# Kernel optimization log

Measured on AMD Instinct MI355X. Metric: run time of the kernel, lower is better.

The kernel has to match this reference:

```python
import jax, jax.numpy as jnp
import numpy as np

# DAttentionBaseline config (matches init_kwargs)
NH, HC, G = 8, 32, 4          # n_heads, n_head_channels, n_groups
ORF = 2.0                      # offset_range_factor
KK = 5                         # offset conv kernel (stage_idx=2)


def _conv1x1(x, w, b=None):
    # x: (B,C,H,W), w: (O,C)
    y = jnp.einsum('bchw,oc->bohw', x, w)
    return y if b is None else y + b[None, :, None, None]


def _ref_points(Hk, Wk, dtype):
    # replicates torch.meshgrid(..., indexing='xy') as in the source
    ly = jnp.linspace(0.5, Hk - 0.5, Hk, dtype=dtype)
    lx = jnp.linspace(0.5, Wk - 0.5, Wk, dtype=dtype)
    ry, rx = jnp.meshgrid(ly, lx, indexing='xy')  # shapes (Wk, Hk); Hk==Wk here
    return jnp.stack([ry / Hk * 2 - 1, rx / Wk * 2 - 1], axis=-1)  # (Hk,Wk,2)


def _grid_sample(img, grid):
    # bilinear, align_corners=True, zero padding. img:(N,C,Hi,Wi), grid:(N,Hg,Wg,2) in [-1,1] (x,y)
    N, C, Hi, Wi = img.shape
    gx = (grid[..., 0] + 1.0) * 0.5 * (Wi - 1)
    gy = (grid[..., 1] + 1.0) * 0.5 * (Hi - 1)
    x0 = jnp.floor(gx); y0 = jnp.floor(gy)
    x1 = x0 + 1.0;      y1 = y0 + 1.0
    wx1 = gx - x0; wx0 = 1.0 - wx1
    wy1 = gy - y0; wy0 = 1.0 - wy1
    nidx = jnp.arange(N)[:, None, None]

    def gather(yf, xf):
        valid = (xf >= 0) & (xf <= Wi - 1) & (yf >= 0) & (yf <= Hi - 1)
        xi = jnp.clip(xf, 0, Wi - 1).astype(jnp.int32)
        yi = jnp.clip(yf, 0, Hi - 1).astype(jnp.int32)
        vals = img[nidx, :, yi, xi]  # (N,Hg,Wg,C)
        return vals * valid[..., None].astype(img.dtype)

    out = (gather(y0, x0) * (wy0 * wx0)[..., None]
           + gather(y0, x1) * (wy0 * wx1)[..., None]
           + gather(y1, x0) * (wy1 * wx0)[..., None]
           + gather(y1, x1) * (wy1 * wx1)[..., None])
    return out.transpose(0, 3, 1, 2)  # (N,C,Hg,Wg)


def _forward(x, wq, bq, w_off_dw, b_off_dw, ln_g, ln_b, w_off_pj, wk, bk, wv, bv, wo, bo, rpe_table):
    B, C, H, W = x.shape
    GC = C // G            # group channels
    GH = NH // G           # group heads
    scale = HC ** -0.5

    q = _conv1x1(x, wq, bq)                                   # (B,C,H,W)
    q_off = q.reshape(B * G, GC, H, W)

    # conv_offset: depthwise conv -> LayerNorm over channels -> GELU -> 1x1 conv to 2
    off = jax.lax.conv_general_dilated(
        q_off, w_off_dw, (1, 1), [(KK // 2, KK // 2), (KK // 2, KK // 2)],
        feature_group_count=GC, dimension_numbers=('NCHW', 'OIHW', 'NCHW'))
    off = off + b_off_dw[None, :, None, None]
    mu = off.mean(axis=1, keepdims=True)
    var = off.var(axis=1, keepdims=True)
    off = (off - mu) * jax.lax.rsqrt(var + 1e-5)
    off = off * ln_g[None, :, None, None] + ln_b[None, :, None, None]
    off = jax.nn.gelu(off, approximate=False)
    offset = jnp.einsum('bchw,oc->bohw', off, w_off_pj)       # (B*G,2,Hk,Wk)

    Hk, Wk = offset.shape[2], offset.shape[3]
    ns = Hk * Wk
    rng = jnp.array([1.0 / Hk, 1.0 / Wk], dtype=x.dtype).reshape(1, 2, 1, 1)
    offset = jnp.tanh(offset) * rng * ORF                     # offset_range_factor > 0
    offset = offset.transpose(0, 2, 3, 1)                     # (B*G,Hk,Wk,2)

    ref = _ref_points(Hk, Wk, x.dtype)                        # (Hk,Wk,2)
    pos = offset + ref[None]                                  # (B*G,Hk,Wk,2), (y,x) order

    xs = _grid_sample(x.reshape(B * G, GC, H, W), pos[..., ::-1])  # (B*G,GC,Hk,Wk)
    xs = xs.reshape(B, C, 1, ns)

    k = _conv1x1(xs, wk, bk).reshape(B * NH, HC, ns)
    v = _conv1x1(xs, wv, bv).reshape(B * NH, HC, ns)
    qf = q.reshape(B * NH, HC, H * W)
    attn = jnp.einsum('bcm,bcn->bmn', qf, k) * scale          # (B*NH, HW, ns)

    # RPE via grid_sample on the (2H-1, 2W-1) bias table
    rpe = jnp.broadcast_to(rpe_table[None], (B,) + rpe_table.shape)
    rpe = rpe.reshape(B * G, GH, 2 * H - 1, 2 * W - 1)
    qg = _ref_points(H, W, x.dtype).reshape(H * W, 2)
    disp = (qg[None, :, None, :] - pos.reshape(B * G, ns, 2)[:, None, :, :]) * 0.5  # (B*G,HW,ns,2)
    bias = _grid_sample(rpe, disp[..., ::-1]).reshape(B * NH, H * W, ns)
    attn = attn + bias

    attn = jax.nn.softmax(attn, axis=2)
    out = jnp.einsum('bmn,bcn->bcm', attn, v).reshape(B, C, H, W)
    y = _conv1x1(out, wo, bo)
    return (y,
            pos.reshape(B, G, Hk, Wk, 2),
            jnp.broadcast_to(ref[None, None], (B, G, Hk, Wk, 2)))


def setup_inputs() -> dict:
    key = jax.random.key(0)
    ks = jax.random.split(key, 8)
    B, C, H, W = 4, 256, 32, 32
    GC = C // G
    s = 0.02

    def n(k, shape, sc=s):
        return jax.random.normal(k, shape, jnp.float32) * sc

    return {
        'x': jax.random.normal(ks[0], (B, C, H, W), jnp.float32),
        'wq': n(ks[1], (C, C)), 'bq': jnp.zeros((C,), jnp.float32),
        'w_off_dw': n(ks[2], (GC, 1, KK, KK)), 'b_off_dw': jnp.zeros((GC,), jnp.float32),
        'ln_g': jnp.ones((GC,), jnp.float32), 'ln_b': jnp.zeros((GC,), jnp.float32),
        'w_off_pj': n(ks[3], (2, GC)),
        'wk': n(ks[4], (C, C)), 'bk': jnp.zeros((C,), jnp.float32),
        'wv': n(ks[5], (C, C)), 'bv': jnp.zeros((C,), jnp.float32),
        'wo': n(ks[6], (C, C)), 'bo': jnp.zeros((C,), jnp.float32),
        'rpe_table': n(ks[7], (NH, 2 * H - 1, 2 * W - 1), 0.01),
    }


def reference(x, wq, bq, w_off_dw, b_off_dw, ln_g, ln_b, w_off_pj, wk, bk, wv, bv, wo, bo, rpe_table):
    return _forward(x, wq, bq, w_off_dw, b_off_dw, ln_g, ln_b, w_off_pj, wk, bk, wv, bv, wo, bo, rpe_table)
```

## Files before the change

### kernel.cpp

```cpp
#include <hip/hip_runtime.h>
#include <math.h>

#define CK __restrict__

constexpr int CH = 256;
constexpr int HW = 1024;

typedef __attribute__((ext_vector_type(8))) short short8;
typedef __attribute__((ext_vector_type(4))) float f32x4;
typedef __attribute__((ext_vector_type(2))) float v2f;

__device__ __forceinline__ ushort f2b(float x) {
    union { float f; unsigned int u; } a; a.f = x;
    unsigned int r = (a.u + 0x7FFFu + ((a.u >> 16) & 1u)) >> 16;
    return (ushort)r;
}
__device__ __forceinline__ short8 ld8(const ushort* p) { return *(const short8*)p; }
__device__ __forceinline__ float u2f(unsigned int u) {
    union { unsigned int u; float f; } a; a.u = u; return a.f;
}
__device__ __forceinline__ float b2f(ushort us) { return u2f((unsigned int)us << 16); }

__global__ __launch_bounds__(256) void prep(const float* CK w0, const float* CK w1,
                                            const float* CK w2, const float* CK w3,
                                            ushort* CK o0, ushort* CK o1,
                                            ushort* CK o2, ushort* CK o3,
                                            const float* CK x, ushort* CK xT,
                                            const float* CK rpe, unsigned int* CK rpetab) {
    const int bid = blockIdx.x, t = threadIdx.x;
    if (bid < 256) {
        const float* src; ushort* dst;
        switch (bid >> 6) {
            case 0: src = w0; dst = o0; break;
            case 1: src = w1; dst = o1; break;
            case 2: src = w2; dst = o2; break;
            default: src = w3; dst = o3; break;
        }
        const int i = (bid & 63) * 256 + t;
        float4 v = ((const float4*)src)[i];
        ushort4 r; r.x = f2b(v.x); r.y = f2b(v.y); r.z = f2b(v.z); r.w = f2b(v.w);
        ((ushort4*)dst)[i] = r;
    } else if (bid < 384) {
        const int b2 = bid - 256;
        const int c8 = b2 & 31, b = b2 >> 5;
        for (int nn = 0; nn < 4; nn++) {
            const int n = nn * 256 + t;
            union { ushort u[8]; short8 s; } pk;
#pragma unroll
            for (int j = 0; j < 8; j++) pk.u[j] = f2b(x[(b * 256 + c8 * 8 + j) * HW + n]);
            *(short8*)(xT + b * 262144 + n * 256 + c8 * 8) = pk.s;
        }
    } else {
        const int h = bid - 384;
        const float* rp = rpe + h * 3969;
        unsigned int* dst = rpetab + h * 4356;
        for (int i = t; i < 4356; i += 256) {
            int y = i / 67, x2 = i - y * 67;
            int yy = y - 1, xx = x2 - 1;
            bool vy = (yy >= 0) && (yy < 63) && (y < 65);
            float a  = (vy && xx >= 0 && xx < 63) ? rp[yy * 63 + xx] : 0.f;
            float bb = (vy && xx >= -1 && xx < 62) ? rp[yy * 63 + xx + 1] : 0.f;
            dst[i] = (unsigned int)f2b(a) | ((unsigned int)f2b(bb) << 16);
        }
    }
}

__global__ __launch_bounds__(256) void gemm_q(const ushort* CK AT, const ushort* CK W,
                                              const float* CK bias, ushort* CK Y) {
    const int bid = blockIdx.x;
    const int my = bid >> 6, b = (bid >> 4) & 3, nx = bid & 15;
    const int t = threadIdx.x, w = t >> 6, l = t & 63;
    const int lm = l & 15, qd = l >> 4;
    const int m0 = my * 64 + (w & 1) * 32;
    const int n0 = nx * 64 + (w >> 1) * 32;
    const ushort* A = AT + b * 262144 + n0 * 256;
    const ushort* Bm = W + m0 * 256;
    f32x4 acc[2][2] = {};
#pragma unroll
    for (int k0 = 0; k0 < 8; k0++) {
        const int ko = k0 * 32 + qd * 8;
        short8 a0 = ld8(A + lm * 256 + ko);
        short8 a1 = ld8(A + (16 + lm) * 256 + ko);
        short8 b0 = ld8(Bm + lm * 256 + ko);
        short8 b1 = ld8(Bm + (16 + lm) * 256 + ko);
        acc[0][0] = __builtin_amdgcn_mfma_f32_16x16x32_bf16(a0, b0, acc[0][0], 0, 0, 0);
        acc[0][1] = __builtin_amdgcn_mfma_f32_16x16x32_bf16(a0, b1, acc[0][1], 0, 0, 0);
        acc[1][0] = __builtin_amdgcn_mfma_f32_16x16x32_bf16(a1, b0, acc[1][0], 0, 0, 0);
        acc[1][1] = __builtin_amdgcn_mfma_f32_16x16x32_bf16(a1, b1, acc[1][1], 0, 0, 0);
    }
#pragma unroll
    for (int in = 0; in < 2; in++)
#pragma unroll
        for (int im = 0; im < 2; im++) {
            const int m = m0 + im * 16 + lm;
            const float bs = bias[m];
            ushort4 r;
            r.x = f2b(acc[in][im][0] + bs); r.y = f2b(acc[in][im][1] + bs);
            r.z = f2b(acc[in][im][2] + bs); r.w = f2b(acc[in][im][3] + bs);
            *(ushort4*)(Y + b * 262144 + m * HW + n0 + in * 16 + qd * 4) = r;
        }
}

__global__ __launch_bounds__(256) void gemm_kv(const ushort* CK AT,
                                               const ushort* CK Wk, const float* CK bk, ushort* CK kbt,
                                               const ushort* CK Wv, const float* CK bv, ushort* CK vbs) {
    const int bid = blockIdx.x;
    const int my = bid >> 6, b = (bid >> 4) & 3, nx = bid & 15;
    const int t = threadIdx.x, w = t >> 6, l = t & 63;
    const int lm = l & 15, qd = l >> 4;
    const int m0 = my * 64 + (w & 1) * 32;
    const int n0 = nx * 64 + (w >> 1) * 32;
    const ushort* A = AT + b * 262144 + n0 * 256;
    const ushort* Bk = Wk + m0 * 256;
    const ushort* Bv = Wv + m0 * 256;
    f32x4 akT[2][2] = {}, av[2][2] = {};
#pragma unroll
    for (int k0 = 0; k0 < 8; k0++) {
        const int ko = k0 * 32 + qd * 8;
        short8 a0 = ld8(A + lm * 256 + ko);
        short8 a1 = ld8(A + (16 + lm) * 256 + ko);
        short8 k0f = ld8(Bk + lm * 256 + ko);
        short8 k1f = ld8(Bk + (16 + lm) * 256 + ko);
        short8 v0f = ld8(Bv + lm * 256 + ko);
        short8 v1f = ld8(Bv + (16 + lm) * 256 + ko);
        akT[0][0] = __builtin_amdgcn_mfma_f32_16x16x32_bf16(k0f, a0, akT[0][0], 0, 0, 0);
        akT[0][1] = __builtin_amdgcn_mfma_f32_16x16x32_bf16(k0f, a1, akT[0][1], 0, 0, 0);
        akT[1][0] = __builtin_amdgcn_mfma_f32_16x16x32_bf16(k1f, a0, akT[1][0], 0, 0, 0);
        akT[1][1] = __builtin_amdgcn_mfma_f32_16x16x32_bf16(k1f, a1, akT[1][1], 0, 0, 0);
        av[0][0] = __builtin_amdgcn_mfma_f32_16x16x32_bf16(a0, v0f, av[0][0], 0, 0, 0);
        av[0][1] = __builtin_amdgcn_mfma_f32_16x16x32_bf16(a0, v1f, av[0][1], 0, 0, 0);
        av[1][0] = __builtin_amdgcn_mfma_f32_16x16x32_bf16(a1, v0f, av[1][0], 0, 0, 0);
        av[1][1] = __builtin_amdgcn_mfma_f32_16x16x32_bf16(a1, v1f, av[1][1], 0, 0, 0);
    }
#pragma unroll
    for (int im = 0; im < 2; im++)
#pragma unroll
        for (int in = 0; in < 2; in++) {
            {
                const int c0 = m0 + im * 16 + qd * 4;
                const int n  = n0 + in * 16 + lm;
                const int bh = b * 8 + (c0 >> 5);
                const int qdk = (c0 & 31) >> 3, co4 = c0 & 7;
                const int nc = n >> 7, nbk = (n >> 4) & 7, lmk = n & 15;
                const float4 bks = *(const float4*)(bk + c0);
                ushort4 r4;
                r4.x = f2b(akT[im][in][0] + bks.x);
                r4.y = f2b(akT[im][in][1] + bks.y);
                r4.z = f2b(akT[im][in][2] + bks.z);
                r4.w = f2b(akT[im][in][3] + bks.w);
                *(ushort4*)(kbt + ((bh * 8 + nc) * 512 + nbk * 64 + qdk * 16 + lmk) * 8 + co4) = r4;
            }
            {
                const int c = m0 + im * 16 + lm;
                const int bh = b * 8 + (c >> 5);
                const float bs = bv[c];
                const int cb = (c & 31) >> 4, lmv = c & 15;
                const int nbase = n0 + in * 16 + qd * 4;
                const int nc = nbase >> 7, kc = (nbase >> 5) & 3;
                const int qdv = (nbase >> 3) & 3, co0 = nbase & 7;
                ushort4 r4;
                r4.x = f2b(av[in][im][0] + bs); r4.y = f2b(av[in][im][1] + bs);
                r4.z = f2b(av[in][im][2] + bs); r4.w = f2b(av[in][im][3] + bs);
                *(ushort4*)(vbs + ((bh * 8 + nc) * 512 + (cb * 4 + kc) * 64 + qdv * 16 + lmv) * 8 + co0) = r4;
            }
        }
}

__global__ __launch_bounds__(256) void dwln(const ushort* CK q, const float* CK wdw,
                                            const float* CK bdw, const float* CK ln_g,
                                            const float* CK ln_b, const float* CK wpj,
                                            const float* CK x,
                                            float* CK out_pos, float* CK out_ref,
                                            float2* CK pos_sc, ushort* CK xsT) {
    __shared__ __align__(16) ushort qs[64 * 218];
    __shared__ __align__(16) float offs[64][68];
    const int bid = blockIdx.x, t = threadIdx.x;
    const int bg = bid & 15, rp = bid >> 4;

    {
        const int ch = t & 63;
        const int r6a = t >> 6;
#pragma unroll
        for (int pass = 0; pass < 2; pass++) {
            const int r6 = (pass == 0) ? r6a : (4 + r6a);
            if (pass == 1 && r6a >= 2) break;
            const int grow = rp * 2 - 2 + r6;
            unsigned int* dst = (unsigned int*)(qs + ch * 218 + r6 * 36);
            if (grow >= 0 && grow <= 31) {
                const unsigned int* src = (const unsigned int*)(q + (bg * 64 + ch) * 1024 + grow * 32);
                dst[0] = 0;
#pragma unroll
                for (int k2 = 0; k2 < 16; k2++) dst[1 + k2] = src[k2];
                dst[17] = 0;
            } else {
#pragma unroll
                for (int k2 = 0; k2 < 18; k2++) dst[k2] = 0;
            }
        }
    }
    __syncthreads();

    {
        const int ch = t >> 2, pg = t & 3;
        const int pr = pg >> 1, c0 = (pg & 1) * 16;
        float w[25];
#pragma unroll
        for (int i = 0; i < 25; i++) w[i] = wdw[ch * 25 + i];
        const float bb = bdw[ch];
        float nb[5][20];
#pragma unroll
        for (int r = 0; r < 5; r++) {
            const unsigned int* row = (const unsigned int*)(qs + ch * 218 + (pr + r) * 36 + c0);
#pragma unroll
            for (int u = 0; u < 10; u++) {
                const unsigned int v = row[u];
                nb[r][u * 2]     = u2f(v << 16);
                nb[r][u * 2 + 1] = u2f(v & 0xFFFF0000u);
            }
        }
#pragma unroll
        for (int j = 0; j < 16; j++) {
            float s = bb;
#pragma unroll
            for (int ky = 0; ky < 5; ky++)
#pragma unroll
                for (int kx = 0; kx < 5; kx++) s += nb[ky][j + kx] * w[ky * 5 + kx];
            offs[pr * 32 + c0 + j][ch] = s;
        }
    }
    __syncthreads();

    const int pix_l = t >> 2, qtr = t & 3;
    const int n = rp * 64 + pix_l;
    const int gid = bg * 1024 + n;
    const int c0 = qtr * 16;
    float v[16];
    {
        const float4* ov = (const float4*)&offs[pix_l][c0];
        const float4 V0 = ov[0], V1 = ov[1], V2 = ov[2], V3 = ov[3];
        v[0] = V0.x;  v[1] = V0.y;  v[2] = V0.z;  v[3] = V0.w;
        v[4] = V1.x;  v[5] = V1.y;  v[6] = V1.z;  v[7] = V1.w;
        v[8] = V2.x;  v[9] = V2.y;  v[10] = V2.z; v[11] = V2.w;
        v[12] = V3.x; v[13] = V3.y; v[14] = V3.z; v[15] = V3.w;
    }
    float s1 = 0.f;
#pragma unroll
    for (int j = 0; j < 16; j++) s1 += v[j];
    s1 += __shfl_xor(s1, 1); s1 += __shfl_xor(s1, 2);
    const float mean = s1 * 0.015625f;
    float s2 = 0.f;
#pragma unroll
    for (int j = 0; j < 16; j++) { float d = v[j] - mean; s2 += d * d; }
    s2 += __shfl_xor(s2, 1); s2 += __shfl_xor(s2, 2);
    const float rs = rsqrtf(s2 * 0.015625f + 1e-5f);
    float p0 = 0.f, p1 = 0.f;
#pragma unroll
    for (int j = 0; j < 16; j++) {
        float vv = (v[j] - mean) * rs * ln_g[c0 + j] + ln_b[c0 + j];
        float gl = 0.5f * vv * (1.f + erff(vv * 0.70710678118654752f));
        p0 += gl * wpj[c0 + j];
        p1 += gl * wpj[64 + c0 + j];
    }
    p0 += __shfl_xor(p0, 1); p0 += __shfl_xor(p0, 2);
    p1 += __shfl_xor(p1, 1); p1 += __shfl_xor(p1, 2);
    const int ii = n >> 5, jj = n & 31;
    const float r0 = (jj + 0.5f) * 0.0625f - 1.f;
    const float r1 = (ii + 0.5f) * 0.0625f - 1.f;
    const float pos0 = tanhf(p0) * 0.0625f + r0;
    const float pos1 = tanhf(p1) * 0.0625f + r1;
    if (qtr == 0) {
        out_pos[gid * 2] = pos0; out_pos[gid * 2 + 1] = pos1;
        out_ref[gid * 2] = r0;   out_ref[gid * 2 + 1] = r1;
        pos_sc[gid].x = pos0 * 15.5f; pos_sc[gid].y = pos1 * 15.5f;
    }
    const float gx = (pos1 + 1.f) * 15.5f, gy = (pos0 + 1.f) * 15.5f;
    const float x0f = floorf(gx), y0f = floorf(gy);
    const float wx1 = gx - x0f, wx0 = 1.f - wx1, wy1 = gy - y0f, wy0 = 1.f - wy1;
    const bool vx0 = (x0f >= 0.f) && (x0f <= 31.f);
    const bool vx1 = (x0f >= -1.f) && (x0f <= 30.f);
    const bool vy0 = (y0f >= 0.f) && (y0f <= 31.f);
    const bool vy1 = (y0f >= -1.f) && (y0f <= 30.f);
    const int xi0 = (int)fminf(fmaxf(x0f, 0.f), 31.f);
    const int xi1 = (int)fminf(fmaxf(x0f + 1.f, 0.f), 31.f);
    const int yi0 = (int)fminf(fmaxf(y0f, 0.f), 31.f);
    const int yi1 = (int)fminf(fmaxf(y0f + 1.f, 0.f), 31.f);
    const float w00 = (vy0 && vx0) ? wy0 * wx0 : 0.f;
    const float w01 = (vy0 && vx1) ? wy0 * wx1 : 0.f;
    const float w10 = (vy1 && vx0) ? wy1 * wx0 : 0.f;
    const float w11 = (vy1 && vx1) ? wy1 * wx1 : 0.f;
    const int o00 = yi0 * 32 + xi0, o01 = yi0 * 32 + xi1;
    const int o10 = yi1 * 32 + xi0, o11 = yi1 * 32 + xi1;
    const int b = bg >> 2, g = bg & 3;
    const float* xb = x + bg * 64 * HW;
    ushort* xo = xsT + b * 262144 + n * 256 + g * 64 + c0;
#pragma unroll
    for (int j4 = 0; j4 < 4; j4++) {
        ushort4 r4;
        float vals[4];
#pragma unroll
        for (int j = 0; j < 4; j++) {
            const float* p = xb + (c0 + j4 * 4 + j) * HW;
            vals[j] = w00 * p[o00] + w01 * p[o01] + w10 * p[o10] + w11 * p[o11];
        }
        r4.x = f2b(vals[0]); r4.y = f2b(vals[1]); r4.z = f2b(vals[2]); r4.w = f2b(vals[3]);
        *(ushort4*)(xo + j4 * 4) = r4;
    }
}

__global__ __launch_bounds__(256, 4) void attn_part(const ushort* CK q, const ushort* CK kbt,
                                                    const ushort* CK vbs, const float2* CK pos_sc,
                                                    const unsigned int* CK rpetab,
                                                    ushort* CK partO, float* CK lbuf) {
    __shared__ __align__(16) unsigned int rpe_pr[4356];
    __shared__ __align__(16) ushort Pl[4][1088];
    const int bid = blockIdx.x;
    const int mt = bid >> 7;
    const int r_ = bid & 127;
    const int bh = r_ >> 2, quarter = r_ & 3;
    const int b = bh >> 3, nh = bh & 7, bg = bh >> 1;
    const int t = threadIdx.x;
    const int w = t >> 6, l = t & 63;
    const int lm = l & 15, qd = l >> 4;

    {
        const uint4* src4 = (const uint4*)(rpetab + nh * 4356);
        uint4* dst4 = (uint4*)rpe_pr;
        for (int i = t; i < 1089; i += 256) dst4[i] = src4[i];
    }
    __syncthreads();

    const int m = mt * 64 + w * 16 + lm;
    short8 qf;
    {
        union { ushort u[8]; short8 s; } pk;
        const ushort* qb = q + (b * 256 + nh * 32) * HW + m;
#pragma unroll
        for (int j = 0; j < 8; j++) pk.u[j] = qb[(qd * 8 + j) * HW];
        qf = pk.s;
    }
    const float qg0 = ((m & 31) + 0.5f) * 0.0625f - 1.f;
    const float qg1 = ((m >> 5) + 0.5f) * 0.0625f - 1.f;
    const float ax = 31.f + 15.5f * qg1;
    const float ay = 31.f + 15.5f * qg0;

    f32x4 oacc0 = {0.f, 0.f, 0.f, 0.f}, oacc1 = {0.f, 0.f, 0.f, 0.f};
    float rsum = 0.f;
    ushort* PlW = Pl[w];
    const float2* pbase = pos_sc + bg * 1024;

    for (int nc = quarter * 2; nc < quarter * 2 + 2; nc++) {
        const ushort* kg = kbt + (bh * 8 + nc) * 4096;
        const ushort* vg = vbs + (bh * 8 + nc) * 4096;

#pragma unroll
        for (int g = 0; g < 2; g++) {
            f32x4 sT[4];
#pragma unroll
            for (int s = 0; s < 4; s++) {
                const int nb = g * 4 + s;
                sT[s] = __builtin_amdgcn_mfma_f32_16x16x32_bf16(
                            ld8(kg + (nb * 64 + l) * 8), qf,
                            (f32x4){0.f, 0.f, 0.f, 0.f}, 0, 0, 0);
            }
#pragma unroll
            for (int s = 0; s < 4; s++) {
                const float4* pp = (const float4*)(pbase + nc * 128 + (g * 4 + s) * 16 + qd * 4);
                const float4 pa = pp[0], pb_ = pp[1];
                const float psx[4] = {pa.x, pa.z, pb_.x, pb_.z};
                const float psy[4] = {pa.y, pa.w, pb_.y, pb_.w};
#pragma unroll
                for (int rp = 0; rp < 2; rp++) {
                    v2f gx = {ax - psy[rp * 2], ax - psy[rp * 2 + 1]};
                    v2f gy = {ay - psx[rp * 2], ay - psx[rp * 2 + 1]};
                    const int xi0 = (int)gx.x, xi1 = (int)gx.y;
                    const int yi0 = (int)gy.x, yi1 = (int)gy.y;
                    v2f wx = gx - (v2f){(float)xi0, (float)xi1};
                    v2f wy = gy - (v2f){(float)yi0, (float)yi1};
                    const int idxA = yi0 * 67 + xi0 + 68;
                    const int idxB = yi1 * 67 + xi1 + 68;
                    const unsigned int a0 = rpe_pr[idxA], a1 = rpe_pr[idxA + 67];
                    const unsigned int b0 = rpe_pr[idxB], b1 = rpe_pr[idxB + 67];
                    v2f tA = {u2f(a0 << 16), u2f(a0 & 0xFFFF0000u)};
                    v2f bA = {u2f(a1 << 16), u2f(a1 & 0xFFFF0000u)};
                    v2f tB = {u2f(b0 << 16), u2f(b0 & 0xFFFF0000u)};
                    v2f bB = {u2f(b1 << 16), u2f(b1 & 0xFFFF0000u)};
                    v2f vA = tA + wy.x * (bA - tA);
                    v2f vB = tB + wy.y * (bB - tB);
                    const float biasA = vA.x + wx.x * (vA.y - vA.x);
                    const float biasB = vB.x + wx.y * (vB.y - vB.x);
                    sT[s][rp * 2]     = sT[s][rp * 2]     * 0.17677669529663687f + biasA;
                    sT[s][rp * 2 + 1] = sT[s][rp * 2 + 1] * 0.17677669529663687f + biasB;
                }
            }
#pragma unroll
            for (int s = 0; s < 4; s++) {
                float e0 = __expf(sT[s][0]);
                float e1 = __expf(sT[s][1]);
                float e2 = __expf(sT[s][2]);
                float e3 = __expf(sT[s][3]);
                rsum += (e0 + e1) + (e2 + e3);
                uint2 pk;
                pk.x = (unsigned int)f2b(e0) | ((unsigned int)f2b(e1) << 16);
                pk.y = (unsigned int)f2b(e2) | ((unsigned int)f2b(e3) << 16);
                *(uint2*)(PlW + s * 272 + l * 4) = pk;
            }
#pragma unroll
            for (int kc = 0; kc < 2; kc++) {
                const ushort* pb2 = PlW + (kc * 2 + (qd >> 1)) * 272 + (qd & 1) * 128 + lm * 4;
                union { uint2 u[2]; short8 s; } pfu;
                pfu.u[0] = *(const uint2*)pb2;
                pfu.u[1] = *(const uint2*)(pb2 + 64);
                const int kv = g * 2 + kc;
                oacc0 = __builtin_amdgcn_mfma_f32_16x16x32_bf16(ld8(vg + (kv * 64 + l) * 8), pfu.s, oacc0, 0, 0, 0);
                oacc1 = __builtin_amdgcn_mfma_f32_16x16x32_bf16(ld8(vg + ((4 + kv) * 64 + l) * 8), pfu.s, oacc1, 0, 0, 0);
            }
        }
    }

    rsum += __shfl_xor(rsum, 16);
    rsum += __shfl_xor(rsum, 32);

    ushort* po = partO + (((quarter * 32 + bh) * 1024 + m) * 32) + qd * 4;
    ushort4 r04, r14;
    r04.x = f2b(oacc0[0]); r04.y = f2b(oacc0[1]); r04.z = f2b(oacc0[2]); r04.w = f2b(oacc0[3]);
    r14.x = f2b(oacc1[0]); r14.y = f2b(oacc1[1]); r14.z = f2b(oacc1[2]); r14.w = f2b(oacc1[3]);
    *(ushort4*)po = r04;
    *(ushort4*)(po + 16) = r14;
    if (qd == 0) lbuf[(quarter * 32 + bh) * 1024 + m] = rsum;
}

__global__ __launch_bounds__(256) void gemm_oc(const ushort* CK partO, const float* CK lbuf,
                                               const ushort* CK W, const float* CK bias,
                                               float* CK Y) {
    __shared__ __align__(16) float ew[64][8];
    const int bid = blockIdx.x;
    const int my = bid >> 6, b = (bid >> 4) & 3, nx = bid & 15;
    const int t = threadIdx.x, w = t >> 6, l = t & 63;
    const int lm = l & 15, qd = l >> 4;
    const int m0 = my * 64 + (w & 1) * 32;
    const int n0 = nx * 64 + (w >> 1) * 32;
    const int nblk = nx * 64;

    for (int p = t; p < 512; p += 256) {
        const int pix = p >> 3, head = p & 7;
        const int mg = nblk + pix;
        const int bh = b * 8 + head;
        float den = 0.f;
#pragma unroll
        for (int q2 = 0; q2 < 4; q2++) den += lbuf[(q2 * 32 + bh) * 1024 + mg];
        ew[pix][head] = 1.f / den;
    }
    __syncthreads();

    const ushort* Bm = W + m0 * 256;
    f32x4 acc[2][2] = {};
#pragma unroll
    for (int k0 = 0; k0 < 8; k0++) {
        const int ko = k0 * 32 + qd * 8;
        short8 af[2];
#pragma unroll
        for (int half = 0; half < 2; half++) {
            const int pix_l = (w >> 1) * 32 + half * 16 + lm;
            const int mg = nblk + pix_l;
            const ushort* pbq = partO + ((b * 8 + k0) * 1024 + mg) * 32 + qd * 8;
            const float inv = ew[pix_l][k0];
            float a8[8] = {};
#pragma unroll
            for (int q2 = 0; q2 < 4; q2++) {
                union { ushort u[8]; short8 s; } pv;
                pv.s = ld8(pbq + q2 * 1048576);
#pragma unroll
                for (int j = 0; j < 8; j++) a8[j] += b2f(pv.u[j]);
            }
            union { ushort u[8]; short8 s; } out;
#pragma unroll
            for (int j = 0; j < 8; j++) out.u[j] = f2b(a8[j] * inv);
            af[half] = out.s;
        }
        short8 b0 = ld8(Bm + lm * 256 + ko);
        short8 b1 = ld8(Bm + (16 + lm) * 256 + ko);
        acc[0][0] = __builtin_amdgcn_mfma_f32_16x16x32_bf16(af[0], b0, acc[0][0], 0, 0, 0);
        acc[0][1] = __builtin_amdgcn_mfma_f32_16x16x32_bf16(af[0], b1, acc[0][1], 0, 0, 0);
        acc[1][0] = __builtin_amdgcn_mfma_f32_16x16x32_bf16(af[1], b0, acc[1][0], 0, 0, 0);
        acc[1][1] = __builtin_amdgcn_mfma_f32_16x16x32_bf16(af[1], b1, acc[1][1], 0, 0, 0);
    }
#pragma unroll
    for (int in = 0; in < 2; in++)
#pragma unroll
        for (int im = 0; im < 2; im++) {
            const int mo = m0 + im * 16 + lm;
            const float bs = bias[mo];
            float4 r;
            r.x = acc[in][im][0] + bs; r.y = acc[in][im][1] + bs;
            r.z = acc[in][im][2] + bs; r.w = acc[in][im][3] + bs;
            *(float4*)(Y + b * 262144 + mo * HW + n0 + in * 16 + qd * 4) = r;
        }
}

extern "C" void kernel_launch(void* const* d_in, const int* in_sizes, int n_in,
                              void* d_out, int out_size, void* d_ws, size_t ws_size,
                              hipStream_t stream) {
    (void)in_sizes; (void)n_in; (void)out_size; (void)ws_size;
    const float* x   = (const float*)d_in[0];
    const float* wq  = (const float*)d_in[1];
    const float* bq  = (const float*)d_in[2];
    const float* wdw = (const float*)d_in[3];
    const float* bdw = (const float*)d_in[4];
    const float* lng = (const float*)d_in[5];
    const float* lnb = (const float*)d_in[6];
    const float* wpj = (const float*)d_in[7];
    const float* wk  = (const float*)d_in[8];
    const float* bk  = (const float*)d_in[9];
    const float* wv  = (const float*)d_in[10];
    const float* bv  = (const float*)d_in[11];
    const float* wo  = (const float*)d_in[12];
    const float* bo  = (const float*)d_in[13];
    const float* rpe = (const float*)d_in[14];
    float* outp = (float*)d_out;
    char* base = (char*)d_ws;
    const size_t MB = 1 << 20;

    ushort* q_b    = (ushort*)(base);
    ushort* kbt    = (ushort*)(base + 2 * MB);
    ushort* vbs    = (ushort*)(base + 4 * MB);
    ushort* xT     = (ushort*)(base + 10 * MB);
    ushort* xsT    = (ushort*)(base + 12 * MB);
    ushort* partO  = (ushort*)(base + 6 * MB);
    float*  lbuf   = (float*)(base + 14 * MB);
    ushort* wqb    = (ushort*)(base + 15 * MB);
    ushort* wkb    = (ushort*)(base + 15 * MB + 131072);
    ushort* wvb    = (ushort*)(base + 15 * MB + 262144);
    ushort* wob    = (ushort*)(base + 15 * MB + 393216);
    float2* pos_sc = (float2*)(base + 15 * MB + 524288);
    unsigned int* rpetab = (unsigned int*)(base + 15 * MB + 655360);

    prep<<<392, 256, 0, stream>>>(wq, wk, wv, wo, wqb, wkb, wvb, wob, x, xT, rpe, rpetab);
    gemm_q<<<256, 256, 0, stream>>>(xT, wqb, bq, q_b);
    dwln<<<256, 256, 0, stream>>>(q_b, wdw, bdw, lng, lnb, wpj, x,
                                  outp + (1 << 20), outp + (1 << 20) + 32768, pos_sc, xsT);
    gemm_kv<<<256, 256, 0, stream>>>(xsT, wkb, bk, kbt, wvb, bv, vbs);
    attn_part<<<2048, 256, 0, stream>>>(q_b, kbt, vbs, pos_sc, rpetab, partO, lbuf);
    gemm_oc<<<256, 256, 0, stream>>>(partO, lbuf, wob, bo, outp);
}
```

Measured before the change: 164.8 us.

## Fold prep kernel into gemm_q and dwln, converting x and wq on the fly

Removes the separate prep launch. gemm_q now reads fp32 x directly, converts and transposes it into shared memory, and converts wq to bf16 in registers as it loads. The conversion of wk/wv/wo and the rpe table padding move into the dwln kernel's prologue. This saves a launch and the xT round trip through memory, in exchange for redundant wq conversion across blocks and a longer dwln prologue.

```diff
diff --git a/kernel.cpp b/kernel.cpp
--- a/kernel.cpp
+++ b/kernel.cpp
@@ -20,74 +20,50 @@
     union { unsigned int u; float f; } a; a.u = u; return a.f;
 }
 __device__ __forceinline__ float b2f(ushort us) { return u2f((unsigned int)us << 16); }
-
-__global__ __launch_bounds__(256) void prep(const float* CK w0, const float* CK w1,
-                                            const float* CK w2, const float* CK w3,
-                                            ushort* CK o0, ushort* CK o1,
-                                            ushort* CK o2, ushort* CK o3,
-                                            const float* CK x, ushort* CK xT,
-                                            const float* CK rpe, unsigned int* CK rpetab) {
-    const int bid = blockIdx.x, t = threadIdx.x;
-    if (bid < 256) {
-        const float* src; ushort* dst;
-        switch (bid >> 6) {
-            case 0: src = w0; dst = o0; break;
-            case 1: src = w1; dst = o1; break;
-            case 2: src = w2; dst = o2; break;
-            default: src = w3; dst = o3; break;
-        }
-        const int i = (bid & 63) * 256 + t;
-        float4 v = ((const float4*)src)[i];
-        ushort4 r; r.x = f2b(v.x); r.y = f2b(v.y); r.z = f2b(v.z); r.w = f2b(v.w);
-        ((ushort4*)dst)[i] = r;
-    } else if (bid < 384) {
-        const int b2 = bid - 256;
-        const int c8 = b2 & 31, b = b2 >> 5;
-        for (int nn = 0; nn < 4; nn++) {
-            const int n = nn * 256 + t;
-            union { ushort u[8]; short8 s; } pk;
-#pragma unroll
-            for (int j = 0; j < 8; j++) pk.u[j] = f2b(x[(b * 256 + c8 * 8 + j) * HW + n]);
-            *(short8*)(xT + b * 262144 + n * 256 + c8 * 8) = pk.s;
-        }
-    } else {
-        const int h = bid - 384;
-        const float* rp = rpe + h * 3969;
-        unsigned int* dst = rpetab + h * 4356;
-        for (int i = t; i < 4356; i += 256) {
-            int y = i / 67, x2 = i - y * 67;
-            int yy = y - 1, xx = x2 - 1;
-            bool vy = (yy >= 0) && (yy < 63) && (y < 65);
-            float a  = (vy && xx >= 0 && xx < 63) ? rp[yy * 63 + xx] : 0.f;
-            float bb = (vy && xx >= -1 && xx < 62) ? rp[yy * 63 + xx + 1] : 0.f;
-            dst[i] = (unsigned int)f2b(a) | ((unsigned int)f2b(bb) << 16);
-        }
-    }
-}
-
-__global__ __launch_bounds__(256) void gemm_q(const ushort* CK AT, const ushort* CK W,
+__device__ __forceinline__ short8 cvt8(const float* CK p) {
+    union { ushort u[8]; short8 s; } r;
+    const float4 v0 = *(const float4*)p, v1 = *(const float4*)(p + 4);
+    r.u[0] = f2b(v0.x); r.u[1] = f2b(v0.y); r.u[2] = f2b(v0.z); r.u[3] = f2b(v0.w);
+    r.u[4] = f2b(v1.x); r.u[5] = f2b(v1.y); r.u[6] = f2b(v1.z); r.u[7] = f2b(v1.w);
+    return r.s;
+}
+
+__global__ __launch_bounds__(256) void gemm_q(const float* CK x, const float* CK wq,
                                               const float* CK bias, ushort* CK Y) {
+    __shared__ __align__(16) ushort xs[64 * 264];
     const int bid = blockIdx.x;
     const int my = bid >> 6, b = (bid >> 4) & 3, nx = bid & 15;
     const int t = threadIdx.x, w = t >> 6, l = t & 63;
     const int lm = l & 15, qd = l >> 4;
+    {
+        const float* src = x + b * 262144 + t * 1024 + nx * 64;
+#pragma unroll
+        for (int j4 = 0; j4 < 16; j4++) {
+            float4 v = *(const float4*)(src + j4 * 4);
+            xs[(j4 * 4 + 0) * 264 + t] = f2b(v.x);
+            xs[(j4 * 4 + 1) * 264 + t] = f2b(v.y);
+            xs[(j4 * 4 + 2) * 264 + t] = f2b(v.z);
+            xs[(j4 * 4 + 3) * 264 + t] = f2b(v.w);
+        }
+    }
+    __syncthreads();
     const int m0 = my * 64 + (w & 1) * 32;
-    const int n0 = nx * 64 + (w >> 1) * 32;
-    const ushort* A = AT + b * 262144 + n0 * 256;
-    const ushort* Bm = W + m0 * 256;
+    const int nl0 = (w >> 1) * 32;
+    const float* Bm = wq + m0 * 256;
     f32x4 acc[2][2] = {};
 #pragma unroll
     for (int k0 = 0; k0 < 8; k0++) {
         const int ko = k0 * 32 + qd * 8;
-        short8 a0 = ld8(A + lm * 256 + ko);
-        short8 a1 = ld8(A + (16 + lm) * 256 + ko);
-        short8 b0 = ld8(Bm + lm * 256 + ko);
-        short8 b1 = ld8(Bm + (16 + lm) * 256 + ko);
+        short8 a0 = ld8(xs + (nl0 + lm) * 264 + ko);
+        short8 a1 = ld8(xs + (nl0 + 16 + lm) * 264 + ko);
+        short8 b0 = cvt8(Bm + lm * 256 + ko);
+        short8 b1 = cvt8(Bm + (16 + lm) * 256 + ko);
         acc[0][0] = __builtin_amdgcn_mfma_f32_16x16x32_bf16(a0, b0, acc[0][0], 0, 0, 0);
         acc[0][1] = __builtin_amdgcn_mfma_f32_16x16x32_bf16(a0, b1, acc[0][1], 0, 0, 0);
         acc[1][0] = __builtin_amdgcn_mfma_f32_16x16x32_bf16(a1, b0, acc[1][0], 0, 0, 0);
         acc[1][1] = __builtin_amdgcn_mfma_f32_16x16x32_bf16(a1, b1, acc[1][1], 0, 0, 0);
     }
+    const int n0 = nx * 64 + nl0;
 #pragma unroll
     for (int in = 0; in < 2; in++)
 #pragma unroll
@@ -170,12 +146,40 @@
                                             const float* CK bdw, const float* CK ln_g,
                                             const float* CK ln_b, const float* CK wpj,
                                             const float* CK x,
+                                            const float* CK wk, const float* CK wv, const float* CK wo,
+                                            ushort* CK wkb, ushort* CK wvb, ushort* CK wob,
+                                            const float* CK rpe, unsigned int* CK rpetab,
                                             float* CK out_pos, float* CK out_ref,
                                             float2* CK pos_sc, ushort* CK xsT) {
     __shared__ __align__(16) ushort qs[64 * 218];
     __shared__ __align__(16) float offs[64][68];
     const int bid = blockIdx.x, t = threadIdx.x;
     const int bg = bid & 15, rp = bid >> 4;
+
+    {
+        const int mat = t >> 6;
+        if (mat < 3) {
+            const float* wsrc = (mat == 0) ? wk : (mat == 1) ? wv : wo;
+            ushort* wdst = (mat == 0) ? wkb : (mat == 1) ? wvb : wob;
+            const int i = bid * 64 + (t & 63);
+            float4 v = ((const float4*)wsrc)[i];
+            ushort4 r; r.x = f2b(v.x); r.y = f2b(v.y); r.z = f2b(v.z); r.w = f2b(v.w);
+            ((ushort4*)wdst)[i] = r;
+        }
+        if (bid >= 248) {
+            const int h = bid - 248;
+            const float* rph = rpe + h * 3969;
+            unsigned int* dst = rpetab + h * 4356;
+            for (int i = t; i < 4356; i += 256) {
+                int y = i / 67, x2 = i - y * 67;
+                int yy = y - 1, xx = x2 - 1;
+                bool vy = (yy >= 0) && (yy < 63) && (y < 65);
+                float a  = (vy && xx >= 0 && xx < 63) ? rph[yy * 63 + xx] : 0.f;
+                float bb = (vy && xx >= -1 && xx < 62) ? rph[yy * 63 + xx + 1] : 0.f;
+                dst[i] = (unsigned int)f2b(a) | ((unsigned int)f2b(bb) << 16);
+            }
+        }
+    }
 
     {
         const int ch = t & 63;
@@ -523,20 +527,18 @@
     ushort* q_b    = (ushort*)(base);
     ushort* kbt    = (ushort*)(base + 2 * MB);
     ushort* vbs    = (ushort*)(base + 4 * MB);
-    ushort* xT     = (ushort*)(base + 10 * MB);
     ushort* xsT    = (ushort*)(base + 12 * MB);
     ushort* partO  = (ushort*)(base + 6 * MB);
     float*  lbuf   = (float*)(base + 14 * MB);
-    ushort* wqb    = (ushort*)(base + 15 * MB);
     ushort* wkb    = (ushort*)(base + 15 * MB + 131072);
     ushort* wvb    = (ushort*)(base + 15 * MB + 262144);
     ushort* wob    = (ushort*)(base + 15 * MB + 393216);
     float2* pos_sc = (float2*)(base + 15 * MB + 524288);
     unsigned int* rpetab = (unsigned int*)(base + 15 * MB + 655360);
 
-    prep<<<392, 256, 0, stream>>>(wq, wk, wv, wo, wqb, wkb, wvb, wob, x, xT, rpe, rpetab);
-    gemm_q<<<256, 256, 0, stream>>>(xT, wqb, bq, q_b);
+    gemm_q<<<256, 256, 0, stream>>>(x, wq, bq, q_b);
     dwln<<<256, 256, 0, stream>>>(q_b, wdw, bdw, lng, lnb, wpj, x,
+                                  wk, wv, wo, wkb, wvb, wob, rpe, rpetab,
                                   outp + (1 << 20), outp + (1 << 20) + 32768, pos_sc, xsT);
     gemm_kv<<<256, 256, 0, stream>>>(xsT, wkb, bk, kbt, wvb, bv, vbs);
     attn_part<<<2048, 256, 0, stream>>>(q_b, kbt, vbs, pos_sc, rpetab, partO, lbuf);
```

Measured after the change: 165.2 us. Within noise of the previous version (+0.3%).
